# Kernel optimization log

Measured on AMD Instinct MI355X. Metric: run time of the kernel, lower is better.

## Reference

```python
import jax, jax.numpy as jnp
import numpy as np

H, C = 4, 32          # heads, per-head channels (hidden_dim = 128)
HID = H * C
NC, NM, E, DIN = 100000, 20000, 400000, 64


def _gat_conv(x_src, x_dst, src, dst, Wsrc, Wdst, asrc, adst, bias):
    """PyG-style bipartite GATConv: gather -> leaky-relu attention -> segment softmax -> scatter."""
    n_dst = x_dst.shape[0]
    hs = (x_src @ Wsrc).reshape(-1, H, C)            # [Ns, H, C]
    hd = (x_dst @ Wdst).reshape(-1, H, C)            # [Nd, H, C]
    a_s = jnp.sum(hs * asrc, axis=-1)                # [Ns, H]
    a_d = jnp.sum(hd * adst, axis=-1)                # [Nd, H]
    e = jax.nn.leaky_relu(a_s[src] + a_d[dst], 0.2)  # [E, H]
    m = jax.ops.segment_max(e, dst, num_segments=n_dst)
    m = jnp.where(jnp.isfinite(m), m, 0.0)           # isolated dst nodes -> -inf max
    ex = jnp.exp(e - m[dst])
    den = jax.ops.segment_sum(ex, dst, num_segments=n_dst)
    alpha = ex / (den[dst] + 1e-16)                  # per-destination segment softmax
    out = jax.ops.segment_sum(hs[src] * alpha[:, :, None], dst, num_segments=n_dst)
    return out.reshape(n_dst, HID) + bias            # concat heads + bias


def _mlp2(x, W1, b1, W2, b2):
    return jax.nn.relu(x @ W1 + b1) @ W2 + b2


def setup_inputs():
    key = jax.random.key(0)
    ks = iter(jax.random.split(key, 80))
    def rn(shape, s):
        return jax.random.normal(next(ks), shape, dtype=jnp.float32) * s
    inp = {}
    inp['x_card'] = rn((NC, DIN), 1.0)
    inp['x_merchant'] = rn((NM, DIN), 1.0)
    for l, din in ((0, DIN), (1, HID)):
        for et in ('cm', 'mc'):
            p = 'l%d_%s_' % (l, et)
            g = (2.0 / (din + HID)) ** 0.5
            inp[p + 'Wsrc'] = rn((din, HID), g)
            inp[p + 'Wdst'] = rn((din, HID), g)
            inp[p + 'asrc'] = rn((H, C), 0.1)
            inp[p + 'adst'] = rn((H, C), 0.1)
            inp[p + 'b'] = jnp.zeros((HID,), jnp.float32)
    for nt in ('card', 'merchant'):
        inp['attw_' + nt] = rn((HID, 1), 0.05)
        inp['attb_' + nt] = jnp.zeros((1,), jnp.float32)
    for nt in ('card', 'mer'):
        inp['cls_%s_W1' % nt] = rn((HID, HID // 2), 0.05)
        inp['cls_%s_b1' % nt] = jnp.zeros((HID // 2,), jnp.float32)
        inp['cls_%s_W2' % nt] = rn((HID // 2, 2), 0.05)
        inp['cls_%s_b2' % nt] = jnp.zeros((2,), jnp.float32)
    inp['risk_W1'] = rn((HID, HID // 2), 0.05)
    inp['risk_b1'] = jnp.zeros((HID // 2,), jnp.float32)
    inp['risk_W2'] = rn((HID // 2, 1), 0.05)
    inp['risk_b2'] = jnp.zeros((1,), jnp.float32)
    inp['cm_src'] = jax.random.randint(next(ks), (E,), 0, NC, dtype=jnp.int32)
    inp['cm_dst'] = jax.random.randint(next(ks), (E,), 0, NM, dtype=jnp.int32)
    inp['mc_src'] = jax.random.randint(next(ks), (E,), 0, NM, dtype=jnp.int32)
    inp['mc_dst'] = jax.random.randint(next(ks), (E,), 0, NC, dtype=jnp.int32)
    return inp


def reference(x_card, x_merchant,
              l0_cm_Wsrc, l0_cm_Wdst, l0_cm_asrc, l0_cm_adst, l0_cm_b,
              l0_mc_Wsrc, l0_mc_Wdst, l0_mc_asrc, l0_mc_adst, l0_mc_b,
              l1_cm_Wsrc, l1_cm_Wdst, l1_cm_asrc, l1_cm_adst, l1_cm_b,
              l1_mc_Wsrc, l1_mc_Wdst, l1_mc_asrc, l1_mc_adst, l1_mc_b,
              attw_card, attb_card, attw_merchant, attb_merchant,
              cls_card_W1, cls_card_b1, cls_card_W2, cls_card_b2,
              cls_mer_W1, cls_mer_b1, cls_mer_W2, cls_mer_b2,
              risk_W1, risk_b1, risk_W2, risk_b2,
              cm_src, cm_dst, mc_src, mc_dst):
    xc, xm = x_card, x_merchant
    # HeteroConv layer 0 (each dst type receives exactly one edge type, so mean-aggr is identity)
    xm1 = _gat_conv(xc, xm, cm_src, cm_dst, l0_cm_Wsrc, l0_cm_Wdst, l0_cm_asrc, l0_cm_adst, l0_cm_b)
    xc1 = _gat_conv(xm, xc, mc_src, mc_dst, l0_mc_Wsrc, l0_mc_Wdst, l0_mc_asrc, l0_mc_adst, l0_mc_b)
    # HeteroConv layer 1
    xm2 = _gat_conv(xc1, xm1, cm_src, cm_dst, l1_cm_Wsrc, l1_cm_Wdst, l1_cm_asrc, l1_cm_adst, l1_cm_b)
    xc2 = _gat_conv(xm1, xc1, mc_src, mc_dst, l1_mc_Wsrc, l1_mc_Wdst, l1_mc_asrc, l1_mc_adst, l1_mc_b)
    # graph-level attention: softmax over the node dimension (dim=0), then reweight
    xc2 = xc2 * jax.nn.softmax(xc2 @ attw_card + attb_card, axis=0)
    xm2 = xm2 * jax.nn.softmax(xm2 @ attw_merchant + attb_merchant, axis=0)
    pred_c = _mlp2(xc2, cls_card_W1, cls_card_b1, cls_card_W2, cls_card_b2)
    pred_m = _mlp2(xm2, cls_mer_W1, cls_mer_b1, cls_mer_W2, cls_mer_b2)
    risk_c = jax.nn.sigmoid(_mlp2(xc2, risk_W1, risk_b1, risk_W2, risk_b2))[:, 0]
    risk_m = jax.nn.sigmoid(_mlp2(xm2, risk_W1, risk_b1, risk_W2, risk_b2))[:, 0]
    return (xc2, xm2, pred_c, pred_m, risk_c, risk_m)
```

## Files before the change

### kernel.cpp

```cpp
#include <hip/hip_runtime.h>

typedef _Float16 f16;
typedef _Float16 f16x2 __attribute__((ext_vector_type(2)));
typedef _Float16 f16x4 __attribute__((ext_vector_type(4)));
typedef _Float16 f16x8 __attribute__((ext_vector_type(8)));
typedef float floatx4 __attribute__((ext_vector_type(4)));

constexpr int NC = 100000;
constexpr int NM = 20000;
constexpr int NE = 400000;

constexpr int OFF_XM2 = NC * 128;
constexpr int OFF_PC  = OFF_XM2 + NM * 128;
constexpr int OFF_PM  = OFF_PC + NC * 2;
constexpr int OFF_RC  = OFF_PM + NM * 2;
constexpr int OFF_RM  = OFF_RC + NC;

__device__ __forceinline__ int bpermi(int v, int srclane) {
  return __builtin_amdgcn_ds_bpermute(srclane << 2, v);
}
__device__ __forceinline__ float bpermf(float v, int srclane) {
  int r = __builtin_amdgcn_ds_bpermute(srclane << 2, __builtin_bit_cast(int, v));
  return __builtin_bit_cast(float, r);
}

__global__ void __launch_bounds__(256) k_prep(
    int* zero_base, int nzero, int* stats_i,
    const float* W0, const float* a0, float* v0,
    const float* W1, const float* a1, float* v1,
    const float* W2, const float* a2, float* v2,
    const float* W3, const float* a3, float* v3,
    const float* cb1, const float* mb1, const float* rb1, float* bC, float* bM,
    const float* S0, const float* S1, const float* S2, const float* S3,
    const float* c1, const float* m1, const float* r1,
    f16* BfL0cm, f16* BfL0mc, f16* BfL1cm, f16* BfL1mc, f16* BfC, f16* BfM) {
  int b = blockIdx.x, t = threadIdx.x;
  if (b < 256) {
    for (int i = b * 256 + t; i < nzero + 4; i += 256 * 256) {
      if (i < nzero) zero_base[i] = 0; else stats_i[i - nzero] = 0;
    }
  } else if (b == 256) {
    const float* Wd[4] = {W0, W1, W2, W3};
    const float* ad[4] = {a0, a1, a2, a3};
    float* vd[4] = {v0, v1, v2, v3};
    for (int idx = t; idx < 1536; idx += 256) {
      int mat, base;
      if (idx < 256)       { mat = 0; base = 0; }
      else if (idx < 512)  { mat = 1; base = 256; }
      else if (idx < 1024) { mat = 2; base = 512; }
      else                 { mat = 3; base = 1024; }
      int local = idx - base, k = local >> 2, h = local & 3;
      const float* W = Wd[mat]; const float* a = ad[mat];
      float s = 0.f;
      for (int c = 0; c < 32; ++c) s += W[k * 128 + h * 32 + c] * a[h * 32 + c];
      vd[mat][local] = s;
    }
    if (t < 128) {
      bC[t] = (t < 64) ? cb1[t] : rb1[t - 64];
      bM[t] = (t < 64) ? mb1[t] : rb1[t - 64];
    }
  } else {
    int s = b - 257;
    const float* Wp = nullptr; const float* cA = nullptr; const float* cB = nullptr;
    f16* dst; int kt;
    if (s < 2)       { Wp = S0; dst = BfL0cm; kt = s; }
    else if (s < 4)  { Wp = S1; dst = BfL0mc; kt = s - 2; }
    else if (s < 8)  { Wp = S2; dst = BfL1cm; kt = s - 4; }
    else if (s < 12) { Wp = S3; dst = BfL1mc; kt = s - 8; }
    else if (s < 16) { cA = c1; cB = r1; dst = BfC; kt = s - 12; }
    else             { cA = m1; cB = r1; dst = BfM; kt = s - 16; }
    for (int e = t; e < 512; e += 256) {
      int lane = e & 63, ct = e >> 6;
      int m = lane & 15, q = lane >> 4;
      int col = ct * 16 + m;
      f16x8 frag;
      #pragma unroll
      for (int j = 0; j < 8; ++j) {
        int k = kt * 32 + q * 8 + j;
        float val = Wp ? Wp[k * 128 + col]
                       : (col < 64 ? cA[k * 64 + col] : cB[k * 64 + (col - 64)]);
        frag[j] = (f16)val;
      }
      *reinterpret_cast<f16x8*>(&dst[(size_t)((kt * 8 + ct) * 64 + lane) * 8]) = frag;
    }
  }
}

__global__ void k_hist(const int* cm_dst, const int* mc_dst, int* cnt_cm, int* cnt_mc) {
  int i = blockIdx.x * blockDim.x + threadIdx.x;
  int stride = gridDim.x * blockDim.x;
  for (; i < NE; i += stride) {
    atomicAdd(&cnt_cm[cm_dst[i]], 1);
    atomicAdd(&cnt_mc[mc_dst[i]], 1);
  }
}

__global__ void __launch_bounds__(256) k_scan1(const int* cnt_cm, const int* cnt_mc,
                                               int* offs_cm, int* offs_mc, int* parts) {
  int b = blockIdx.x;
  const int* cnt; int* offs; int n, chunk;
  if (b < 20) { cnt = cnt_cm; offs = offs_cm; n = NM; chunk = b; }
  else        { cnt = cnt_mc; offs = offs_mc; n = NC; chunk = b - 20; }
  int t = threadIdx.x;
  int base = chunk * 1024;
  int v[4]; int tsum = 0;
  #pragma unroll
  for (int j = 0; j < 4; ++j) {
    int idx = base + t * 4 + j;
    v[j] = (idx < n) ? cnt[idx] : 0;
    tsum += v[j];
  }
  __shared__ int sd[256];
  sd[t] = tsum; __syncthreads();
  for (int off = 1; off < 256; off <<= 1) {
    int x = (t >= off) ? sd[t - off] : 0;
    __syncthreads();
    sd[t] += x;
    __syncthreads();
  }
  int excl = sd[t] - tsum;
  int r = excl;
  #pragma unroll
  for (int j = 0; j < 4; ++j) {
    int idx = base + t * 4 + j;
    if (idx < n) offs[idx] = r;
    r += v[j];
  }
  if (t == 0) parts[b] = sd[255];
}

__global__ void __launch_bounds__(256) k_scan2(int* parts) {
  int b = blockIdx.x;
  int base = (b == 0) ? 0 : 20;
  int n = (b == 0) ? 20 : 98;
  int t = threadIdx.x;
  __shared__ int sd[128];
  int v = 0;
  if (t < 128) { v = (t < n) ? parts[base + t] : 0; sd[t] = v; }
  __syncthreads();
  for (int off = 1; off < 128; off <<= 1) {
    int x = 0;
    if (t < 128 && t >= off) x = sd[t - off];
    __syncthreads();
    if (t < 128) sd[t] += x;
    __syncthreads();
  }
  if (t < 128 && t < n) parts[base + t] = sd[t] - v;
}

__global__ void k_scan3(int* offs_cm, int* offs_mc, int* cur_cm, int* cur_mc, const int* parts) {
  int i = blockIdx.x * blockDim.x + threadIdx.x;
  if (i < NM) {
    int val = offs_cm[i] + parts[i >> 10];
    offs_cm[i] = val; cur_cm[i] = val;
  } else if (i < NM + NC) {
    int j = i - NM;
    int val = offs_mc[j] + parts[20 + (j >> 10)];
    offs_mc[j] = val; cur_mc[j] = val;
  }
  if (i == 0) { offs_cm[NM] = NE; offs_mc[NC] = NE; }
}

__global__ void k_scatter(const int* cm_src, const int* cm_dst,
                          const int* mc_src, const int* mc_dst,
                          int* cur_cm, int* cur_mc, int* csr_cm, int* csr_mc) {
  int i = blockIdx.x * blockDim.x + threadIdx.x;
  int stride = gridDim.x * blockDim.x;
  for (; i < NE; i += stride) {
    int p = atomicAdd(&cur_cm[cm_dst[i]], 1);
    csr_cm[p] = cm_src[i];
    int q = atomicAdd(&cur_mc[mc_dst[i]], 1);
    csr_mc[q] = mc_src[i];
  }
}

struct GemmSide {
  const float* x; const f16* Bf;
  const float* asrc; const float* v; f16* hs; float* asO; float* adO;
  const float* bias; const float* wnum; const float* den; float* outx;
  const float* W2; const float* B2; const float* w2r; const float* b2r;
  float* pred; float* risk;
  int M;
};

template<int K, int EPI>
__global__ void __launch_bounds__(256) k_gemm(GemmSide A, GemmSide B, int gridA) {
  constexpr int PP = K + 8;
  constexpr int F4 = K / 4;
  __shared__ f16 xs16[64 * PP];
  const bool isA = (int)blockIdx.x < gridA;
  GemmSide S = isA ? A : B;
  const int blk = isA ? (int)blockIdx.x : (int)blockIdx.x - gridA;
  const int rows0 = blk * 64;
  const int t = (int)threadIdx.x;
  float invden_s = 0.f;
  if constexpr (EPI == 1) invden_s = 1.0f / S.den[0];
  const float4* x4 = reinterpret_cast<const float4*>(S.x);
  #pragma unroll
  for (int ii = 0; ii < (64 * F4) / 256; ++ii) {
    int idx = t + ii * 256;
    int r = idx / F4, f = idx % F4;
    int gr = rows0 + r;
    float4 val = {0.f, 0.f, 0.f, 0.f};
    if (gr < S.M) val = x4[(size_t)gr * F4 + f];
    f16x4 hv; hv.x = (f16)val.x; hv.y = (f16)val.y; hv.z = (f16)val.z; hv.w = (f16)val.w;
    *reinterpret_cast<f16x4*>(&xs16[r * PP + f * 4]) = hv;
    if constexpr (EPI == 1) {
      if (gr < S.M) {
        float w = S.wnum[gr] * invden_s;
        float4 ov = {val.x * w, val.y * w, val.z * w, val.w * w};
        *reinterpret_cast<float4*>(&S.outx[(size_t)gr * 128 + f * 4]) = ov;
      }
    }
  }
  __syncthreads();
  const int lane = t & 63, w = t >> 6;
  const int m = lane & 15, q = lane >> 4;
  const int rbase = w * 16;
  floatx4 acc[8];
  #pragma unroll
  for (int ct = 0; ct < 8; ++ct) acc[ct] = {0.f, 0.f, 0.f, 0.f};
  const f16x8* Bf8 = reinterpret_cast<const f16x8*>(S.Bf);
  #pragma unroll
  for (int kt = 0; kt < K / 32; ++kt) {
    f16x8 a = *reinterpret_cast<const f16x8*>(&xs16[(rbase + m) * PP + kt * 32 + q * 8]);
    #pragma unroll
    for (int ct = 0; ct < 8; ++ct) {
      f16x8 b = Bf8[(kt * 8 + ct) * 64 + lane];
      acc[ct] = __builtin_amdgcn_mfma_f32_16x16x32_f16(a, b, acc[ct], 0, 0, 0);
    }
  }
  if constexpr (EPI == 0) {
    #pragma unroll
    for (int reg = 0; reg < 4; ++reg) {
      int gr = rows0 + rbase + q * 4 + reg;
      bool ok = gr < S.M;
      #pragma unroll
      for (int cp = 0; cp < 4; ++cp) {
        float v0 = acc[2 * cp][reg], v1 = acc[2 * cp + 1][reg];
        float w0 = __shfl_xor(v0, 1), w1 = __shfl_xor(v1, 1);
        bool even = (m & 1) == 0;
        f16x2 pr;
        pr.x = (f16)(even ? v0 : w1);
        pr.y = (f16)(even ? w0 : v1);
        int col = even ? (2 * cp) * 16 + m : (2 * cp + 1) * 16 + m - 1;
        if (ok) *reinterpret_cast<f16x2*>(&S.hs[(size_t)gr * 128 + col]) = pr;
      }
    }
    float as0[4], as1[4];
    #pragma unroll
    for (int h = 0; h < 4; ++h) { as0[h] = S.asrc[h * 32 + m]; as1[h] = S.asrc[h * 32 + 16 + m]; }
    #pragma unroll
    for (int reg = 0; reg < 4; ++reg) {
      float p[4];
      #pragma unroll
      for (int h = 0; h < 4; ++h)
        p[h] = acc[2 * h][reg] * as0[h] + acc[2 * h + 1][reg] * as1[h];
      #pragma unroll
      for (int off = 1; off < 16; off <<= 1) {
        #pragma unroll
        for (int h = 0; h < 4; ++h) p[h] += __shfl_xor(p[h], off);
      }
      int gr = rows0 + rbase + q * 4 + reg;
      if (m == 0 && gr < S.M) {
        float4 pv = {p[0], p[1], p[2], p[3]};
        *reinterpret_cast<float4*>(&S.asO[gr * 4]) = pv;
      }
    }
    float qd[4] = {0.f, 0.f, 0.f, 0.f};
    const float4* v4p = reinterpret_cast<const float4*>(S.v);
    constexpr int KS = K / 4;
    #pragma unroll
    for (int i = 0; i < KS; ++i) {
      int k = q * KS + i;
      float xv = (float)xs16[(rbase + m) * PP + k];
      float4 vk = v4p[k];
      qd[0] += xv * vk.x; qd[1] += xv * vk.y; qd[2] += xv * vk.z; qd[3] += xv * vk.w;
    }
    #pragma unroll
    for (int h = 0; h < 4; ++h) {
      qd[h] += __shfl_xor(qd[h], 16);
      qd[h] += __shfl_xor(qd[h], 32);
    }
    int gr2 = rows0 + rbase + m;
    if (q == 0 && gr2 < S.M) {
      float4 qv = {qd[0], qd[1], qd[2], qd[3]};
      *reinterpret_cast<float4*>(&S.adO[gr2 * 4]) = qv;
    }
  } else {
    float wn[4];
    #pragma unroll
    for (int reg = 0; reg < 4; ++reg) {
      int gr = rows0 + rbase + q * 4 + reg;
      wn[reg] = (gr < S.M) ? S.wnum[gr] * invden_s : 0.f;
    }
    float bct[8], w2c0[4], w2c1[4], w2rv[4];
    #pragma unroll
    for (int ct = 0; ct < 8; ++ct) bct[ct] = S.bias[ct * 16 + m];
    #pragma unroll
    for (int ct = 0; ct < 4; ++ct) {
      int col = ct * 16 + m;
      w2c0[ct] = S.W2[col * 2];
      w2c1[ct] = S.W2[col * 2 + 1];
      w2rv[ct] = S.w2r[col];
    }
    #pragma unroll
    for (int reg = 0; reg < 4; ++reg) {
      float p0 = 0.f, p1 = 0.f, rr = 0.f;
      #pragma unroll
      for (int ct = 0; ct < 4; ++ct) {
        float hv = fmaxf(acc[ct][reg] * wn[reg] + bct[ct], 0.f);
        p0 += hv * w2c0[ct];
        p1 += hv * w2c1[ct];
      }
      #pragma unroll
      for (int ct = 4; ct < 8; ++ct) {
        float hv = fmaxf(acc[ct][reg] * wn[reg] + bct[ct], 0.f);
        rr += hv * w2rv[ct - 4];
      }
      #pragma unroll
      for (int off = 1; off < 16; off <<= 1) {
        p0 += __shfl_xor(p0, off);
        p1 += __shfl_xor(p1, off);
        rr += __shfl_xor(rr, off);
      }
      int gr = rows0 + rbase + q * 4 + reg;
      if (m == 0 && gr < S.M) {
        float2 pp = {p0 + S.B2[0], p1 + S.B2[1]};
        *reinterpret_cast<float2*>(&S.pred[gr * 2]) = pp;
        float z = rr + S.b2r[0];
        S.risk[gr] = 1.f / (1.f + __expf(-z));
      }
    }
  }
}

struct AggSide {
  const int* offs; const int* csr; const float* as_; const float* ad;
  const f16* hs; const float* bias; float* out;
  const float* attw; const float* attb; float* logv;
};

__global__ void __launch_bounds__(256) k_agg(AggSide A, AggSide B, int ndstA, int ntot) {
  const int wid = (int)blockIdx.x * 4 + ((int)threadIdx.x >> 6);
  if (wid >= ntot) return;
  const bool isA = wid < ndstA;
  const AggSide S = isA ? A : B;
  const int d = isA ? wid : wid - ndstA;
  const int lane = (int)threadIdx.x & 63;
  const int we = lane >> 2, wh = lane & 3;
  const int gh = lane >> 4;
  const int beg = S.offs[d], end = S.offs[d + 1];
  const float adv = S.ad[d * 4 + wh];
  const f16* __restrict__ hsp = S.hs;
  float m_run = -1e30f, den = 0.f;
  float accx = 0.f, accy = 0.f;
  for (int base = beg; base < end; base += 16) {
    const int n = min(16, end - base);
    int s = 0; float e = -1e30f;
    if (we < n) {
      s = S.csr[base + we];
      float ev = S.as_[s * 4 + wh] + adv;
      e = (ev > 0.f) ? ev : 0.2f * ev;
    }
    float cm = e;
    #pragma unroll
    for (int msk = 4; msk < 64; msk <<= 1) cm = fmaxf(cm, __shfl_xor(cm, msk));
    const float m_new = fmaxf(m_run, cm);
    const float scale = __expf(m_run - m_new);
    const float w = __expf(e - m_new);
    float ws = w;
    #pragma unroll
    for (int msk = 4; msk < 64; msk <<= 1) ws += __shfl_xor(ws, msk);
    den = den * scale + ws;
    m_run = m_new;
    const float sg = bpermf(scale, gh);
    accx *= sg; accy *= sg;
    int j = 0;
    for (; j + 4 <= n; j += 4) {
      int s0 = bpermi(s, (j + 0) * 4);
      int s1 = bpermi(s, (j + 1) * 4);
      int s2 = bpermi(s, (j + 2) * 4);
      int s3 = bpermi(s, (j + 3) * 4);
      float w0 = bpermf(w, (j + 0) * 4 + gh);
      float w1 = bpermf(w, (j + 1) * 4 + gh);
      float w2 = bpermf(w, (j + 2) * 4 + gh);
      float w3 = bpermf(w, (j + 3) * 4 + gh);
      f16x2 h0 = *reinterpret_cast<const f16x2*>(&hsp[s0 * 128 + lane * 2]);
      f16x2 h1 = *reinterpret_cast<const f16x2*>(&hsp[s1 * 128 + lane * 2]);
      f16x2 h2 = *reinterpret_cast<const f16x2*>(&hsp[s2 * 128 + lane * 2]);
      f16x2 h3 = *reinterpret_cast<const f16x2*>(&hsp[s3 * 128 + lane * 2]);
      accx += w0 * (float)h0.x + w1 * (float)h1.x + w2 * (float)h2.x + w3 * (float)h3.x;
      accy += w0 * (float)h0.y + w1 * (float)h1.y + w2 * (float)h2.y + w3 * (float)h3.y;
    }
    for (; j < n; ++j) {
      int sj = bpermi(s, j * 4);
      float wj = bpermf(w, j * 4 + gh);
      f16x2 hj = *reinterpret_cast<const f16x2*>(&hsp[sj * 128 + lane * 2]);
      accx += wj * (float)hj.x;
      accy += wj * (float)hj.y;
    }
  }
  const float deng = bpermf(den, gh);
  const float invden = (deng > 0.f) ? 1.f / deng : 0.f;
  const float2 b2 = *reinterpret_cast<const float2*>(&S.bias[lane * 2]);
  float ox = accx * invden + b2.x;
  float oy = accy * invden + b2.y;
  float2 o = {ox, oy};
  *reinterpret_cast<float2*>(&S.out[d * 128 + lane * 2]) = o;
  if (S.attw) {
    float sl = ox * S.attw[lane * 2] + oy * S.attw[lane * 2 + 1];
    #pragma unroll
    for (int msk = 1; msk < 64; msk <<= 1) sl += __shfl_xor(sl, msk);
    if (lane == 0) S.logv[d] = sl + S.attb[0];
  }
}

__global__ void __launch_bounds__(1024) k_stats(const float* logc, const float* logm, float* stats) {
  const float* src = (blockIdx.x == 0) ? logc : logm;
  int n = (blockIdx.x == 0) ? NC : NM;
  float m = -1e30f;
  for (int i = threadIdx.x; i < n; i += 1024) m = fmaxf(m, src[i]);
  __shared__ float sd[1024];
  sd[threadIdx.x] = m; __syncthreads();
  for (int off = 512; off > 0; off >>= 1) {
    if ((int)threadIdx.x < off) sd[threadIdx.x] = fmaxf(sd[threadIdx.x], sd[threadIdx.x + off]);
    __syncthreads();
  }
  if (threadIdx.x == 0) stats[blockIdx.x] = sd[0];
}

__global__ void __launch_bounds__(256) k_expsum(float* logc, float* logm, float* stats) {
  bool card = (int)blockIdx.x < 256;
  float* logv = card ? logc : logm;
  int n = card ? NC : NM;
  float mx = card ? stats[0] : stats[1];
  int b0 = card ? (int)blockIdx.x : (int)blockIdx.x - 256;
  int nb = card ? 256 : 64;
  float local = 0.f;
  for (int i = b0 * 256 + (int)threadIdx.x; i < n; i += nb * 256) {
    float e = __expf(logv[i] - mx);
    logv[i] = e;
    local += e;
  }
  __shared__ float sd[256];
  sd[threadIdx.x] = local; __syncthreads();
  for (int off = 128; off > 0; off >>= 1) {
    if ((int)threadIdx.x < off) sd[threadIdx.x] += sd[threadIdx.x + off];
    __syncthreads();
  }
  if (threadIdx.x == 0) atomicAdd(card ? &stats[2] : &stats[3], sd[0]);
}

extern "C" void kernel_launch(void* const* d_in, const int* in_sizes, int n_in,
                              void* d_out, int out_size, void* d_ws, size_t ws_size,
                              hipStream_t stream) {
  (void)in_sizes; (void)n_in; (void)out_size; (void)ws_size;
  const float* x_card    = (const float*)d_in[0];
  const float* x_mer     = (const float*)d_in[1];
  const float* l0cm_Wsrc = (const float*)d_in[2];
  const float* l0cm_Wdst = (const float*)d_in[3];
  const float* l0cm_asrc = (const float*)d_in[4];
  const float* l0cm_adst = (const float*)d_in[5];
  const float* l0cm_b    = (const float*)d_in[6];
  const float* l0mc_Wsrc = (const float*)d_in[7];
  const float* l0mc_Wdst = (const float*)d_in[8];
  const float* l0mc_asrc = (const float*)d_in[9];
  const float* l0mc_adst = (const float*)d_in[10];
  const float* l0mc_b    = (const float*)d_in[11];
  const float* l1cm_Wsrc = (const float*)d_in[12];
  const float* l1cm_Wdst = (const float*)d_in[13];
  const float* l1cm_asrc = (const float*)d_in[14];
  const float* l1cm_adst = (const float*)d_in[15];
  const float* l1cm_b    = (const float*)d_in[16];
  const float* l1mc_Wsrc = (const float*)d_in[17];
  const float* l1mc_Wdst = (const float*)d_in[18];
  const float* l1mc_asrc = (const float*)d_in[19];
  const float* l1mc_adst = (const float*)d_in[20];
  const float* l1mc_b    = (const float*)d_in[21];
  const float* attw_c    = (const float*)d_in[22];
  const float* attb_c    = (const float*)d_in[23];
  const float* attw_m    = (const float*)d_in[24];
  const float* attb_m    = (const float*)d_in[25];
  const float* clsc_W1   = (const float*)d_in[26];
  const float* clsc_b1   = (const float*)d_in[27];
  const float* clsc_W2   = (const float*)d_in[28];
  const float* clsc_b2   = (const float*)d_in[29];
  const float* clsm_W1   = (const float*)d_in[30];
  const float* clsm_b1   = (const float*)d_in[31];
  const float* clsm_W2   = (const float*)d_in[32];
  const float* clsm_b2   = (const float*)d_in[33];
  const float* risk_W1   = (const float*)d_in[34];
  const float* risk_b1   = (const float*)d_in[35];
  const float* risk_W2   = (const float*)d_in[36];
  const float* risk_b2   = (const float*)d_in[37];
  const int*   cm_src    = (const int*)d_in[38];
  const int*   cm_dst    = (const int*)d_in[39];
  const int*   mc_src    = (const int*)d_in[40];
  const int*   mc_dst    = (const int*)d_in[41];
  float* out = (float*)d_out;

  float* base = (float*)d_ws;
  size_t o = 0;
  auto alloc = [&](size_t n) { float* p = base + o; o += (n + 3) & ~size_t(3); return p; };
  float* hs_card = alloc((size_t)NC * 128);
  float* xc1     = alloc((size_t)NC * 128);
  float* hs_mer  = alloc((size_t)NM * 128);
  float* xm1     = alloc((size_t)NM * 128);
  float* as_card = alloc((size_t)NC * 4);
  float* ad_card = alloc((size_t)NC * 4);
  float* as_mer  = alloc((size_t)NM * 4);
  float* ad_mer  = alloc((size_t)NM * 4);
  float* v_l0cm  = alloc(512);
  float* v_l0mc  = alloc(512);
  float* v_l1cm  = alloc(512);
  float* v_l1mc  = alloc(512);
  float* bC      = alloc(128);
  float* bM      = alloc(128);
  f16* Bf_l0cm = (f16*)alloc(64 * 128 / 2);
  f16* Bf_l0mc = (f16*)alloc(64 * 128 / 2);
  f16* Bf_l1cm = (f16*)alloc(128 * 128 / 2);
  f16* Bf_l1mc = (f16*)alloc(128 * 128 / 2);
  f16* Bf_catC = (f16*)alloc(128 * 128 / 2);
  f16* Bf_catM = (f16*)alloc(128 * 128 / 2);
  float* logc    = alloc(NC);
  float* logm    = alloc(NM);
  float* stats   = alloc(4);
  int* cnt_cm  = (int*)alloc(NM);
  int* cnt_mc  = (int*)alloc(NC);
  int* offs_cm = (int*)alloc(NM + 1);
  int* offs_mc = (int*)alloc(NC + 1);
  int* cur_cm  = (int*)alloc(NM);
  int* cur_mc  = (int*)alloc(NC);
  int* parts   = (int*)alloc(128);
  int* csr_cm  = (int*)alloc(NE);
  int* csr_mc  = (int*)alloc(NE);

  const dim3 B256(256);
  k_prep<<<dim3(277), B256, 0, stream>>>(
      cnt_cm, NM + NC, (int*)stats,
      l0cm_Wdst, l0cm_adst, v_l0cm, l0mc_Wdst, l0mc_adst, v_l0mc,
      l1cm_Wdst, l1cm_adst, v_l1cm, l1mc_Wdst, l1mc_adst, v_l1mc,
      clsc_b1, clsm_b1, risk_b1, bC, bM,
      l0cm_Wsrc, l0mc_Wsrc, l1cm_Wsrc, l1mc_Wsrc,
      clsc_W1, clsm_W1, risk_W1,
      Bf_l0cm, Bf_l0mc, Bf_l1cm, Bf_l1mc, Bf_catC, Bf_catM);
  k_hist<<<dim3(512), B256, 0, stream>>>(cm_dst, mc_dst, cnt_cm, cnt_mc);
  k_scan1<<<dim3(118), B256, 0, stream>>>(cnt_cm, cnt_mc, offs_cm, offs_mc, parts);
  k_scan2<<<dim3(2), B256, 0, stream>>>(parts);
  k_scan3<<<dim3(469), B256, 0, stream>>>(offs_cm, offs_mc, cur_cm, cur_mc, parts);
  k_scatter<<<dim3(512), B256, 0, stream>>>(cm_src, cm_dst, mc_src, mc_dst,
                                            cur_cm, cur_mc, csr_cm, csr_mc);
  const int gA = (NC + 63) / 64;
  const int gB = (NM + 63) / 64;
  const int NTOT = NM + NC;
  const int gAgg = (NTOT + 3) / 4;

  GemmSide sA, sB;
  AggSide aA, aB;
  sA = {x_card, Bf_l0cm, l0cm_asrc, v_l0mc, (f16*)hs_card, as_card, ad_card,
        nullptr, nullptr, nullptr, nullptr, nullptr, nullptr, nullptr, nullptr,
        nullptr, nullptr, NC};
  sB = {x_mer, Bf_l0mc, l0mc_asrc, v_l0cm, (f16*)hs_mer, as_mer, ad_mer,
        nullptr, nullptr, nullptr, nullptr, nullptr, nullptr, nullptr, nullptr,
        nullptr, nullptr, NM};
  k_gemm<64, 0><<<dim3(gA + gB), B256, 0, stream>>>(sA, sB, gA);
  aA = {offs_cm, csr_cm, as_card, ad_mer, (const f16*)hs_card, l0cm_b, xm1,
        nullptr, nullptr, nullptr};
  aB = {offs_mc, csr_mc, as_mer, ad_card, (const f16*)hs_mer, l0mc_b, xc1,
        nullptr, nullptr, nullptr};
  k_agg<<<dim3(gAgg), B256, 0, stream>>>(aA, aB, NM, NTOT);
  sA = {xc1, Bf_l1cm, l1cm_asrc, v_l1mc, (f16*)hs_card, as_card, ad_card,
        nullptr, nullptr, nullptr, nullptr, nullptr, nullptr, nullptr, nullptr,
        nullptr, nullptr, NC};
  sB = {xm1, Bf_l1mc, l1mc_asrc, v_l1cm, (f16*)hs_mer, as_mer, ad_mer,
        nullptr, nullptr, nullptr, nullptr, nullptr, nullptr, nullptr, nullptr,
        nullptr, nullptr, NM};
  k_gemm<128, 0><<<dim3(gA + gB), B256, 0, stream>>>(sA, sB, gA);
  aA = {offs_cm, csr_cm, as_card, ad_mer, (const f16*)hs_card, l1cm_b, xm1,
        attw_m, attb_m, logm};
  aB = {offs_mc, csr_mc, as_mer, ad_card, (const f16*)hs_mer, l1mc_b, xc1,
        attw_c, attb_c, logc};
  k_agg<<<dim3(gAgg), B256, 0, stream>>>(aA, aB, NM, NTOT);
  k_stats<<<dim3(2), dim3(1024), 0, stream>>>(logc, logm, stats);
  k_expsum<<<dim3(320), B256, 0, stream>>>(logc, logm, stats);
  sA = {xc1, Bf_catC, nullptr, nullptr, nullptr, nullptr, nullptr,
        bC, logc, stats + 2, out,
        clsc_W2, clsc_b2, risk_W2, risk_b2,
        out + OFF_PC, out + OFF_RC, NC};
  sB = {xm1, Bf_catM, nullptr, nullptr, nullptr, nullptr, nullptr,
        bM, logm, stats + 3, out + OFF_XM2,
        clsm_W2, clsm_b2, risk_W2, risk_b2,
        out + OFF_PM, out + OFF_RM, NM};
  k_gemm<128, 1><<<dim3(gA + gB), B256, 0, stream>>>(sA, sB, gA);
}
```

Measured before the change: 510.0 us.

## Store intermediate node features in fp16 and widen aggregation loads to 8 bytes

The aggregation kernel now writes the layer outputs xc1/xm1 in fp16 instead of fp32, and the later GEMMs read fp16 input directly through a new IN16 template path. This halves the intermediate write and re-read traffic. The aggregation loop is also reorganized so each half-wave handles alternate edges with 4-channel f16x4 loads, and the two halves are combined with a cross-half shuffle at the end. The cost is reduced precision in the layer-1 inputs and in the final xc2/xm2 values, which are derived from the fp16 copies.

```diff
diff --git a/kernel.cpp b/kernel.cpp
--- a/kernel.cpp
+++ b/kernel.cpp
@@ -175,7 +175,7 @@
 }
 
 struct GemmSide {
-  const float* x; const f16* Bf;
+  const void* x; const f16* Bf;
   const float* asrc; const float* v; f16* hs; float* asO; float* adO;
   const float* bias; const float* wnum; const float* den; float* outx;
   const float* W2; const float* B2; const float* w2r; const float* b2r;
@@ -183,10 +183,9 @@
   int M;
 };
 
-template<int K, int EPI>
+template<int K, int EPI, bool IN16>
 __global__ void __launch_bounds__(256) k_gemm(GemmSide A, GemmSide B, int gridA) {
   constexpr int PP = K + 8;
-  constexpr int F4 = K / 4;
   __shared__ f16 xs16[64 * PP];
   const bool isA = (int)blockIdx.x < gridA;
   GemmSide S = isA ? A : B;
@@ -195,21 +194,45 @@
   const int t = (int)threadIdx.x;
   float invden_s = 0.f;
   if constexpr (EPI == 1) invden_s = 1.0f / S.den[0];
-  const float4* x4 = reinterpret_cast<const float4*>(S.x);
-  #pragma unroll
-  for (int ii = 0; ii < (64 * F4) / 256; ++ii) {
-    int idx = t + ii * 256;
-    int r = idx / F4, f = idx % F4;
-    int gr = rows0 + r;
-    float4 val = {0.f, 0.f, 0.f, 0.f};
-    if (gr < S.M) val = x4[(size_t)gr * F4 + f];
-    f16x4 hv; hv.x = (f16)val.x; hv.y = (f16)val.y; hv.z = (f16)val.z; hv.w = (f16)val.w;
-    *reinterpret_cast<f16x4*>(&xs16[r * PP + f * 4]) = hv;
-    if constexpr (EPI == 1) {
-      if (gr < S.M) {
-        float w = S.wnum[gr] * invden_s;
-        float4 ov = {val.x * w, val.y * w, val.z * w, val.w * w};
-        *reinterpret_cast<float4*>(&S.outx[(size_t)gr * 128 + f * 4]) = ov;
+  if constexpr (!IN16) {
+    constexpr int F4 = K / 4;
+    const float4* x4 = reinterpret_cast<const float4*>(S.x);
+    #pragma unroll
+    for (int ii = 0; ii < (64 * F4) / 256; ++ii) {
+      int idx = t + ii * 256;
+      int r = idx / F4, f = idx % F4;
+      int gr = rows0 + r;
+      float4 val = {0.f, 0.f, 0.f, 0.f};
+      if (gr < S.M) val = x4[(size_t)gr * F4 + f];
+      f16x4 hv; hv.x = (f16)val.x; hv.y = (f16)val.y; hv.z = (f16)val.z; hv.w = (f16)val.w;
+      *reinterpret_cast<f16x4*>(&xs16[r * PP + f * 4]) = hv;
+      if constexpr (EPI == 1) {
+        if (gr < S.M) {
+          float w = S.wnum[gr] * invden_s;
+          float4 ov = {val.x * w, val.y * w, val.z * w, val.w * w};
+          *reinterpret_cast<float4*>(&S.outx[(size_t)gr * 128 + f * 4]) = ov;
+        }
+      }
+    }
+  } else {
+    constexpr int F8 = K / 8;
+    const f16x8* x8 = reinterpret_cast<const f16x8*>(S.x);
+    #pragma unroll
+    for (int ii = 0; ii < (64 * F8) / 256; ++ii) {
+      int idx = t + ii * 256;
+      int r = idx / F8, f = idx % F8;
+      int gr = rows0 + r;
+      f16x8 val = {0, 0, 0, 0, 0, 0, 0, 0};
+      if (gr < S.M) val = x8[(size_t)gr * F8 + f];
+      *reinterpret_cast<f16x8*>(&xs16[r * PP + f * 8]) = val;
+      if constexpr (EPI == 1) {
+        if (gr < S.M) {
+          float w = S.wnum[gr] * invden_s;
+          float4 o1 = {(float)val[0] * w, (float)val[1] * w, (float)val[2] * w, (float)val[3] * w};
+          float4 o2 = {(float)val[4] * w, (float)val[5] * w, (float)val[6] * w, (float)val[7] * w};
+          *reinterpret_cast<float4*>(&S.outx[(size_t)gr * 128 + f * 8]) = o1;
+          *reinterpret_cast<float4*>(&S.outx[(size_t)gr * 128 + f * 8 + 4]) = o2;
+        }
       }
     }
   }
@@ -337,7 +360,7 @@
 
 struct AggSide {
   const int* offs; const int* csr; const float* as_; const float* ad;
-  const f16* hs; const float* bias; float* out;
+  const f16* hs; const float* bias; f16* out;
   const float* attw; const float* attb; float* logv;
 };
 
@@ -349,12 +372,13 @@
   const int d = isA ? wid : wid - ndstA;
   const int lane = (int)threadIdx.x & 63;
   const int we = lane >> 2, wh = lane & 3;
-  const int gh = lane >> 4;
+  const int h2 = lane >> 5, cl = lane & 31;
+  const int gh = cl >> 3;
   const int beg = S.offs[d], end = S.offs[d + 1];
   const float adv = S.ad[d * 4 + wh];
   const f16* __restrict__ hsp = S.hs;
   float m_run = -1e30f, den = 0.f;
-  float accx = 0.f, accy = 0.f;
+  floatx4 acc = {0.f, 0.f, 0.f, 0.f};
   for (int base = beg; base < end; base += 16) {
     const int n = min(16, end - base);
     int s = 0; float e = -1e30f;
@@ -375,44 +399,52 @@
     den = den * scale + ws;
     m_run = m_new;
     const float sg = bpermf(scale, gh);
-    accx *= sg; accy *= sg;
-    int j = 0;
-    for (; j + 4 <= n; j += 4) {
-      int s0 = bpermi(s, (j + 0) * 4);
-      int s1 = bpermi(s, (j + 1) * 4);
-      int s2 = bpermi(s, (j + 2) * 4);
-      int s3 = bpermi(s, (j + 3) * 4);
-      float w0 = bpermf(w, (j + 0) * 4 + gh);
-      float w1 = bpermf(w, (j + 1) * 4 + gh);
-      float w2 = bpermf(w, (j + 2) * 4 + gh);
-      float w3 = bpermf(w, (j + 3) * 4 + gh);
-      f16x2 h0 = *reinterpret_cast<const f16x2*>(&hsp[s0 * 128 + lane * 2]);
-      f16x2 h1 = *reinterpret_cast<const f16x2*>(&hsp[s1 * 128 + lane * 2]);
-      f16x2 h2 = *reinterpret_cast<const f16x2*>(&hsp[s2 * 128 + lane * 2]);
-      f16x2 h3 = *reinterpret_cast<const f16x2*>(&hsp[s3 * 128 + lane * 2]);
-      accx += w0 * (float)h0.x + w1 * (float)h1.x + w2 * (float)h2.x + w3 * (float)h3.x;
-      accy += w0 * (float)h0.y + w1 * (float)h1.y + w2 * (float)h2.y + w3 * (float)h3.y;
-    }
-    for (; j < n; ++j) {
+    acc.x *= sg; acc.y *= sg; acc.z *= sg; acc.w *= sg;
+    int jb = 0;
+    for (; jb + 4 <= n; jb += 4) {
+      int sa = bpermi(s, (jb + h2) * 4);
+      int sb = bpermi(s, (jb + h2 + 2) * 4);
+      float wa = bpermf(w, (jb + h2) * 4 + gh);
+      float wb = bpermf(w, (jb + h2 + 2) * 4 + gh);
+      f16x4 ha = *reinterpret_cast<const f16x4*>(&hsp[sa * 128 + cl * 4]);
+      f16x4 hb = *reinterpret_cast<const f16x4*>(&hsp[sb * 128 + cl * 4]);
+      acc.x += wa * (float)ha.x + wb * (float)hb.x;
+      acc.y += wa * (float)ha.y + wb * (float)hb.y;
+      acc.z += wa * (float)ha.z + wb * (float)hb.z;
+      acc.w += wa * (float)ha.w + wb * (float)hb.w;
+    }
+    for (int j = jb + h2; j < n; j += 2) {
       int sj = bpermi(s, j * 4);
       float wj = bpermf(w, j * 4 + gh);
-      f16x2 hj = *reinterpret_cast<const f16x2*>(&hsp[sj * 128 + lane * 2]);
-      accx += wj * (float)hj.x;
-      accy += wj * (float)hj.y;
-    }
-  }
+      f16x4 hj = *reinterpret_cast<const f16x4*>(&hsp[sj * 128 + cl * 4]);
+      acc.x += wj * (float)hj.x;
+      acc.y += wj * (float)hj.y;
+      acc.z += wj * (float)hj.z;
+      acc.w += wj * (float)hj.w;
+    }
+  }
+  acc.x += __shfl_xor(acc.x, 32);
+  acc.y += __shfl_xor(acc.y, 32);
+  acc.z += __shfl_xor(acc.z, 32);
+  acc.w += __shfl_xor(acc.w, 32);
   const float deng = bpermf(den, gh);
   const float invden = (deng > 0.f) ? 1.f / deng : 0.f;
-  const float2 b2 = *reinterpret_cast<const float2*>(&S.bias[lane * 2]);
-  float ox = accx * invden + b2.x;
-  float oy = accy * invden + b2.y;
-  float2 o = {ox, oy};
-  *reinterpret_cast<float2*>(&S.out[d * 128 + lane * 2]) = o;
+  const float4 b4 = *reinterpret_cast<const float4*>(&S.bias[cl * 4]);
+  float o0 = acc.x * invden + b4.x;
+  float o1 = acc.y * invden + b4.y;
+  float o2 = acc.z * invden + b4.z;
+  float o3 = acc.w * invden + b4.w;
   if (S.attw) {
-    float sl = ox * S.attw[lane * 2] + oy * S.attw[lane * 2 + 1];
-    #pragma unroll
-    for (int msk = 1; msk < 64; msk <<= 1) sl += __shfl_xor(sl, msk);
+    const float4 aw = *reinterpret_cast<const float4*>(&S.attw[cl * 4]);
+    float sl = o0 * aw.x + o1 * aw.y + o2 * aw.z + o3 * aw.w;
+    #pragma unroll
+    for (int msk = 1; msk < 32; msk <<= 1) sl += __shfl_xor(sl, msk);
     if (lane == 0) S.logv[d] = sl + S.attb[0];
+  }
+  if (h2 == 0) {
+    f16x4 ov;
+    ov.x = (f16)o0; ov.y = (f16)o1; ov.z = (f16)o2; ov.w = (f16)o3;
+    *reinterpret_cast<f16x4*>(&S.out[d * 128 + cl * 4]) = ov;
   }
 }
 
@@ -503,10 +535,10 @@
   float* base = (float*)d_ws;
   size_t o = 0;
   auto alloc = [&](size_t n) { float* p = base + o; o += (n + 3) & ~size_t(3); return p; };
-  float* hs_card = alloc((size_t)NC * 128);
-  float* xc1     = alloc((size_t)NC * 128);
-  float* hs_mer  = alloc((size_t)NM * 128);
-  float* xm1     = alloc((size_t)NM * 128);
+  f16* hs_card = (f16*)alloc((size_t)NC * 64);
+  f16* xc1     = (f16*)alloc((size_t)NC * 64);
+  f16* hs_mer  = (f16*)alloc((size_t)NM * 64);
+  f16* xm1     = (f16*)alloc((size_t)NM * 64);
   float* as_card = alloc((size_t)NC * 4);
   float* ad_card = alloc((size_t)NC * 4);
   float* as_mer  = alloc((size_t)NM * 4);
@@ -558,28 +590,28 @@
 
   GemmSide sA, sB;
   AggSide aA, aB;
-  sA = {x_card, Bf_l0cm, l0cm_asrc, v_l0mc, (f16*)hs_card, as_card, ad_card,
+  sA = {x_card, Bf_l0cm, l0cm_asrc, v_l0mc, hs_card, as_card, ad_card,
         nullptr, nullptr, nullptr, nullptr, nullptr, nullptr, nullptr, nullptr,
         nullptr, nullptr, NC};
-  sB = {x_mer, Bf_l0mc, l0mc_asrc, v_l0cm, (f16*)hs_mer, as_mer, ad_mer,
+  sB = {x_mer, Bf_l0mc, l0mc_asrc, v_l0cm, hs_mer, as_mer, ad_mer,
         nullptr, nullptr, nullptr, nullptr, nullptr, nullptr, nullptr, nullptr,
         nullptr, nullptr, NM};
-  k_gemm<64, 0><<<dim3(gA + gB), B256, 0, stream>>>(sA, sB, gA);
-  aA = {offs_cm, csr_cm, as_card, ad_mer, (const f16*)hs_card, l0cm_b, xm1,
+  k_gemm<64, 0, false><<<dim3(gA + gB), B256, 0, stream>>>(sA, sB, gA);
+  aA = {offs_cm, csr_cm, as_card, ad_mer, hs_card, l0cm_b, xm1,
         nullptr, nullptr, nullptr};
-  aB = {offs_mc, csr_mc, as_mer, ad_card, (const f16*)hs_mer, l0mc_b, xc1,
+  aB = {offs_mc, csr_mc, as_mer, ad_card, hs_mer, l0mc_b, xc1,
         nullptr, nullptr, nullptr};
   k_agg<<<dim3(gAgg), B256, 0, stream>>>(aA, aB, NM, NTOT);
-  sA = {xc1, Bf_l1cm, l1cm_asrc, v_l1mc, (f16*)hs_card, as_card, ad_card,
+  sA = {xc1, Bf_l1cm, l1cm_asrc, v_l1mc, hs_card, as_card, ad_card,
         nullptr, nullptr, nullptr, nullptr, nullptr, nullptr, nullptr, nullptr,
         nullptr, nullptr, NC};
-  sB = {xm1, Bf_l1mc, l1mc_asrc, v_l1cm, (f16*)hs_mer, as_mer, ad_mer,
+  sB = {xm1, Bf_l1mc, l1mc_asrc, v_l1cm, hs_mer, as_mer, ad_mer,
         nullptr, nullptr, nullptr, nullptr, nullptr, nullptr, nullptr, nullptr,
         nullptr, nullptr, NM};
-  k_gemm<128, 0><<<dim3(gA + gB), B256, 0, stream>>>(sA, sB, gA);
-  aA = {offs_cm, csr_cm, as_card, ad_mer, (const f16*)hs_card, l1cm_b, xm1,
+  k_gemm<128, 0, true><<<dim3(gA + gB), B256, 0, stream>>>(sA, sB, gA);
+  aA = {offs_cm, csr_cm, as_card, ad_mer, hs_card, l1cm_b, xm1,
         attw_m, attb_m, logm};
-  aB = {offs_mc, csr_mc, as_mer, ad_card, (const f16*)hs_mer, l1mc_b, xc1,
+  aB = {offs_mc, csr_mc, as_mer, ad_card, hs_mer, l1mc_b, xc1,
         attw_c, attb_c, logc};
   k_agg<<<dim3(gAgg), B256, 0, stream>>>(aA, aB, NM, NTOT);
   k_stats<<<dim3(2), dim3(1024), 0, stream>>>(logc, logm, stats);
@@ -592,5 +624,5 @@
         bM, logm, stats + 3, out + OFF_XM2,
         clsm_W2, clsm_b2, risk_W2, risk_b2,
         out + OFF_PM, out + OFF_RM, NM};
-  k_gemm<128, 1><<<dim3(gA + gB), B256, 0, stream>>>(sA, sB, gA);
-}
+  k_gemm<128, 1, true><<<dim3(gA + gB), B256, 0, stream>>>(sA, sB, gA);
+}
```

Result: no change. 510.3 us (+0.1%).
